# Kernel tuning notes

Measured on AMD Instinct MI355X. Metric: run time of the kernel, lower is better.

## Reference

```python
import jax, jax.numpy as jnp
import numpy as np

EMBED = 1024
N_HEAD = 16
D_HID = EMBED // N_HEAD
R_FF = 4
D_FF = EMBED * R_FF
LN_EPS = 1e-5


def layer_norm(x, gamma, beta):
    mu = jnp.mean(x, axis=-1, keepdims=True)
    var = jnp.var(x, axis=-1, keepdims=True)
    return (x - mu) * jax.lax.rsqrt(var + LN_EPS) * gamma + beta


def setup_inputs() -> dict:
    key = jax.random.key(0)
    ks = jax.random.split(key, 10)
    B, S = 4, 2048
    # torch nn.Linear stores weight as [out, in]; y = x @ W.T
    def xavier(k, shape):
        fan_out, fan_in = shape
        lim = np.sqrt(6.0 / (fan_in + fan_out))
        return jax.random.uniform(k, shape, jnp.float32, -lim, lim)
    return {
        "x": jax.random.normal(ks[0], (B, S, EMBED), jnp.float32),
        "Wq": xavier(ks[1], (EMBED, EMBED)),
        "Wk": xavier(ks[2], (EMBED, EMBED)),
        "Wv": xavier(ks[3], (EMBED, EMBED)),
        "Wo": xavier(ks[4], (EMBED, EMBED)),
        "bo": jnp.zeros((EMBED,), jnp.float32),
        "ln1_g": jnp.ones((EMBED,), jnp.float32),
        "ln1_b": jnp.zeros((EMBED,), jnp.float32),
        "ln2_g": jnp.ones((EMBED,), jnp.float32),
        "ln2_b": jnp.zeros((EMBED,), jnp.float32),
        "W1": jax.random.normal(ks[5], (D_FF, EMBED), jnp.float32) * np.sqrt(2.0 / EMBED),
        "b1": jnp.zeros((D_FF,), jnp.float32),
        "W2": xavier(ks[6], (EMBED, D_FF)),
        "b2": jnp.zeros((EMBED,), jnp.float32),
    }


def reference(x, Wq, Wk, Wv, Wo, bo, ln1_g, ln1_b, ln2_g, ln2_b, W1, b1, W2, b2):
    B, S, E = x.shape
    scaling = 1.0 / np.sqrt(D_HID)
    # --- attention (pre-LN), dropout = identity (eval) ---
    xn = layer_norm(x, ln1_g, ln1_b)
    q = (xn @ Wq.T).reshape(B, S, N_HEAD, D_HID) * scaling
    k = (xn @ Wk.T).reshape(B, S, N_HEAD, D_HID)
    v = (xn @ Wv.T).reshape(B, S, N_HEAD, D_HID)
    scores = jnp.einsum("bqhd,bkhd->bhqk", q, k)
    attn = jax.nn.softmax(scores, axis=-1)
    out = jnp.einsum("bhqk,bkhd->bqhd", attn, v).reshape(B, S, E)
    out = out @ Wo.T + bo
    x = x + out
    # --- feed-forward (pre-LN) ---
    xn = layer_norm(x, ln2_g, ln2_b)
    h = jax.nn.relu(xn @ W1.T + b1)
    x = x + (h @ W2.T + b2)
    return x
```

## Files before the change

kernel.cpp:

```cpp
#include <hip/hip_runtime.h>
#include <hip/hip_bf16.h>
#include <cstdint>


typedef __attribute__((ext_vector_type(8))) short bf16x8;
typedef __attribute__((ext_vector_type(4))) float f32x4;

#define LDSAS __attribute__((address_space(3)))
#define GLBAS __attribute__((address_space(1)))

#define CQK 0.18033688011112044f

__device__ __forceinline__ unsigned short f2bf(float f) {
  union { float f; unsigned u; } c; c.f = f;
  unsigned u = c.u + 0x7fffu + ((c.u >> 16) & 1u);
  return (unsigned short)(u >> 16);
}

__device__ __forceinline__ unsigned pk2(float a, float b) {
  __hip_bfloat162 h = __float22bfloat162_rn(make_float2(a, b));
  union { __hip_bfloat162 h; unsigned u; } c; c.h = h; return c.u;
}

__device__ __forceinline__ void async16(const unsigned short* g, unsigned short* l) {
  __builtin_amdgcn_global_load_lds((const GLBAS unsigned int*)g,
                                   (LDSAS unsigned int*)l, 16, 0, 0);
}

__global__ void cvt_all(const float* __restrict__ q, const float* __restrict__ k,
                        const float* __restrict__ v, const float* __restrict__ o,
                        const float* __restrict__ w1, const float* __restrict__ w2,
                        unsigned short* __restrict__ wsb) {
  const long i = (long)blockIdx.x * 256 + threadIdx.x;
  const float* src; unsigned short* dst; long off;
  if (i < 1048576) {
    const long seg = i >> 18, o4 = i & 262143;
    src = (seg == 0) ? q : (seg == 1) ? k : (seg == 2) ? v : o;
    dst = wsb + ((seg == 3) ? 3145728L : seg * 1048576L);
    off = o4;
  } else if (i < 2097152) {
    src = w1; dst = wsb + 4194304; off = i - 1048576;
  } else {
    src = w2; dst = wsb + 8388608; off = i - 2097152;
  }
  const float4 vv = ((const float4*)src)[off];
  ushort4 r;
  r.x = f2bf(vv.x); r.y = f2bf(vv.y); r.z = f2bf(vv.z); r.w = f2bf(vv.w);
  ((ushort4*)dst)[off] = r;
}

__global__ void ln_fwd(const float* __restrict__ x, const float* __restrict__ g,
                       const float* __restrict__ bb, unsigned short* __restrict__ outp) {
  const int row = blockIdx.x, tid = threadIdx.x;
  const float4 v = ((const float4*)(x + (long)row * 1024))[tid];
  float s  = v.x + v.y + v.z + v.w;
  float sq = v.x * v.x + v.y * v.y + v.z * v.z + v.w * v.w;
#pragma unroll
  for (int off = 1; off < 64; off <<= 1) {
    s  += __shfl_xor(s, off);
    sq += __shfl_xor(sq, off);
  }
  __shared__ float red[8];
  const int wv = tid >> 6, lane = tid & 63;
  if (lane == 0) { red[wv] = s; red[4 + wv] = sq; }
  __syncthreads();
  s  = red[0] + red[1] + red[2] + red[3];
  sq = red[4] + red[5] + red[6] + red[7];
  const float mu  = s * (1.f / 1024.f);
  const float var = sq * (1.f / 1024.f) - mu * mu;
  const float rstd = rsqrtf(var + 1e-5f);
  const float4 gv = ((const float4*)g)[tid];
  const float4 bv = ((const float4*)bb)[tid];
  ushort4 o;
  o.x = f2bf((v.x - mu) * rstd * gv.x + bv.x);
  o.y = f2bf((v.y - mu) * rstd * gv.y + bv.y);
  o.z = f2bf((v.z - mu) * rstd * gv.z + bv.z);
  o.w = f2bf((v.w - mu) * rstd * gv.w + bv.w);
  ((ushort4*)(outp + (long)row * 1024))[tid] = o;
}

template <int EPI>
__launch_bounds__(256, 3)
__global__ void gemm_bt(const unsigned short* __restrict__ A,
                        const unsigned short* __restrict__ B,
                        void* __restrict__ Cout,
                        const float* __restrict__ bias,
                        const float* __restrict__ res,
                        int M, int N, int K) {
  __shared__ __align__(16) unsigned short As[128 * 64];
  __shared__ __align__(16) unsigned short Bs[128 * 64];
  const int tid  = threadIdx.x;
  const int lane = tid & 63;
  const int wvu  = __builtin_amdgcn_readfirstlane(tid >> 6);
  const int quad = lane >> 4, l16 = lane & 15;
  const int wm = wvu >> 1, wn = wvu & 1;

  const int gx = gridDim.x;
  const int id = blockIdx.y * gx + blockIdx.x;
  const int xcd = id & 7, slot = id >> 3;
  const int by = xcd * 8 + (slot & 7);
  const int bx = slot >> 3;
  const long m0 = (long)by * 128, n0 = (long)bx * 128;

  f32x4 acc[4][4];
#pragma unroll
  for (int i = 0; i < 4; i++)
#pragma unroll
    for (int j = 0; j < 4; j++) acc[i][j] = (f32x4){0.f, 0.f, 0.f, 0.f};

  const int rxA = l16 & 7;
  const int c0A = quad ^ rxA;
  int srow[4], sgc[4];
#pragma unroll
  for (int j = 0; j < 4; ++j) {
    const int s = wvu * 256 + j * 64 + lane;
    srow[j] = s >> 3;
    sgc[j] = ((s & 7) ^ (srow[j] & 7)) * 8;
  }

  for (int k0 = 0; k0 < K; k0 += 64) {
    __syncthreads();
#pragma unroll
    for (int j = 0; j < 4; ++j) {
      const int db = (wvu * 256 + j * 64) * 8;
      async16(A + (m0 + srow[j]) * K + k0 + sgc[j], As + db);
      async16(B + (n0 + srow[j]) * K + k0 + sgc[j], Bs + db);
    }
    __syncthreads();

#pragma unroll
    for (int kc = 0; kc < 2; ++kc) {
      const int ch = (c0A ^ (kc * 4)) * 8;
      bf16x8 af[4], bfr[4];
#pragma unroll
      for (int t = 0; t < 4; ++t) {
        af[t]  = *(const bf16x8*)(As + (wm * 64 + t * 16 + l16) * 64 + ch);
        bfr[t] = *(const bf16x8*)(Bs + (wn * 64 + t * 16 + l16) * 64 + ch);
      }
#pragma unroll
      for (int mt = 0; mt < 4; ++mt)
#pragma unroll
        for (int nt = 0; nt < 4; ++nt)
          acc[mt][nt] = __builtin_amdgcn_mfma_f32_16x16x32_bf16(af[mt], bfr[nt],
                                                                acc[mt][nt], 0, 0, 0);
    }
  }

#pragma unroll
  for (int nt = 0; nt < 4; ++nt) {
    const long col = n0 + wn * 64 + nt * 16 + l16;
    float bv = 0.f;
    if (EPI == 1 || EPI == 2) bv = bias[col];
    const float scl = (EPI == 3 && col < 1024) ? CQK : 1.0f;
#pragma unroll
    for (int mt = 0; mt < 4; ++mt) {
#pragma unroll
      for (int r = 0; r < 4; ++r) {
        const long row = m0 + wm * 64 + mt * 16 + quad * 4 + r;
        const long idx = row * (long)N + col;
        float v = acc[mt][nt][r];
        if (EPI == 0) {
          ((unsigned short*)Cout)[idx] = f2bf(v);
        } else if (EPI == 1) {
          ((float*)Cout)[idx] = v + bv + res[idx];
        } else if (EPI == 2) {
          v += bv;
          ((unsigned short*)Cout)[idx] = f2bf(v > 0.f ? v : 0.f);
        } else {
          ((unsigned short*)Cout)[idx] = f2bf(v * scl);
        }
      }
    }
  }
}

__global__ void vprep(const unsigned short* __restrict__ qkv,
                      unsigned short* __restrict__ vt) {
  __shared__ unsigned short T[64 * 68];
  const int tid = threadIdx.x;
  const int t = blockIdx.x;
  const int bh = blockIdx.y;
  const int b = bh >> 4, h = bh & 15;
  const long base = ((long)b * 2048 + t * 64) * 3072 + 2048 + h * 64;
#pragma unroll
  for (int i = 0; i < 4; ++i) {
    int c = i * 256 + tid;
    int r = c >> 4, d4 = (c & 15) * 4;
    *(ushort4*)(T + r * 68 + d4) = *(const ushort4*)(qkv + base + (long)r * 3072 + d4);
  }
  __syncthreads();
  unsigned short* out = vt + ((long)bh * 32 + t) * 4096;
#pragma unroll
  for (int i = 0; i < 4; ++i) {
    int u = i * 256 + tid;
    int c = u >> 1, half = u & 1;
    int d = c >> 3;
    int k = ((c & 7) - d) & 7;
    int kvp4 = k * 8 + half * 4;
    int sk = (kvp4 & 32) | ((kvp4 & 4) << 2) | ((kvp4 & 16) >> 1) | ((kvp4 & 8) >> 1);
    ushort4 o;
    o.x = T[(sk + 0) * 68 + d];
    o.y = T[(sk + 1) * 68 + d];
    o.z = T[(sk + 2) * 68 + d];
    o.w = T[(sk + 3) * 68 + d];
    *(ushort4*)(out + u * 4) = o;
  }
}

__launch_bounds__(256, 2)
__global__ void attn_fwd(const unsigned short* __restrict__ qkv,
                         const unsigned short* __restrict__ vt,
                         unsigned short* __restrict__ outp) {
  __shared__ __align__(16) unsigned short lds[32768];

  const int tid = threadIdx.x;
  const int lane = tid & 63;
  const int wv = __builtin_amdgcn_readfirstlane(tid >> 6);
  const int quad = lane >> 4, l16 = lane & 15;

  const int id = blockIdx.y * 16 + blockIdx.x;
  const int xcd = id & 7, slot = id >> 3;
  const int bh = xcd * 8 + (slot >> 4);
  const int qt = slot & 15;
  const int b = bh >> 4, h = bh & 15;
  const long rowbase = (long)b * 2048;
  const int hoff = h * 64;

  unsigned short* Qs = lds + 16384;

  {
    const unsigned short* qsrc = qkv + (rowbase + qt * 128) * 3072 + hoff;
#pragma unroll
    for (int j = 0; j < 4; ++j) {
      const int c = j * 256 + wv * 64 + lane;
      const int row = c >> 3;
      const int k = ((c & 7) - row) & 7;
      async16(qsrc + (long)row * 3072 + k * 8, Qs + (j * 256 + wv * 64) * 8);
    }
  }
  asm volatile("s_waitcnt vmcnt(0)" ::: "memory");
  __builtin_amdgcn_s_barrier();
  __builtin_amdgcn_sched_barrier(0);

  const int rot0 = (quad + l16) & 7;
  const int rot1 = rot0 ^ 4;

  bf16x8 bq[2][2];
#pragma unroll
  for (int s = 0; s < 2; ++s) {
    const int qrow = wv * 32 + s * 16 + l16;
    bq[s][0] = *(const bf16x8*)(Qs + qrow * 64 + rot0 * 8);
    bq[s][1] = *(const bf16x8*)(Qs + qrow * 64 + rot1 * 8);
  }
  asm volatile("s_waitcnt lgkmcnt(0)" ::: "memory");
  __builtin_amdgcn_sched_barrier(0);
  __builtin_amdgcn_s_barrier();
  __builtin_amdgcn_sched_barrier(0);

  const int c0 = wv * 64 + lane;
  const int r0 = c0 >> 3;
  const int ks = ((c0 & 7) - r0) & 7;
  const unsigned short* kptr = qkv + (rowbase + r0) * 3072 + 1024 + hoff + ks * 8;
  const unsigned short* vptr = vt + (long)bh * 131072 + (long)c0 * 8;

  auto stage = [&](int t) {
    unsigned short* kdst = lds + (t & 1) * 16384 + wv * 512;
    unsigned short* vdst = kdst + 8192;
    const unsigned short* kp = kptr + (long)t * 128 * 3072;
    const unsigned short* vp = vptr + (long)t * 8192;
#pragma unroll
    for (int j = 0; j < 4; ++j) {
      async16(kp + (long)j * 32 * 3072, kdst + j * 2048);
      async16(vp + j * 2048, vdst + j * 2048);
    }
  };

  bf16x8 ones;
#pragma unroll
  for (int i = 0; i < 8; ++i) ones[i] = (short)0x3F80;

  f32x4 oacc[2][4], lacc[2];
#pragma unroll
  for (int s = 0; s < 2; ++s) {
    lacc[s] = (f32x4){0.f, 0.f, 0.f, 0.f};
#pragma unroll
    for (int i = 0; i < 4; ++i) oacc[s][i] = (f32x4){0.f, 0.f, 0.f, 0.f};
  }

  stage(0); stage(1);
  asm volatile("s_waitcnt vmcnt(8)" ::: "memory");
  __builtin_amdgcn_s_barrier();
  __builtin_amdgcn_sched_barrier(0);

  for (int kt = 0; kt < 16; ++kt) {
    const unsigned short* Kb = lds + (kt & 1) * 16384;
    const unsigned short* Vb = Kb + 8192;

    f32x4 sacc[2][8];
#pragma unroll
    for (int t = 0; t < 8; ++t) {
      const int ar = t * 16 + l16;
      bf16x8 ak0 = *(const bf16x8*)(Kb + ar * 64 + rot0 * 8);
      bf16x8 ak1 = *(const bf16x8*)(Kb + ar * 64 + rot1 * 8);
#pragma unroll
      for (int s = 0; s < 2; ++s) {
        f32x4 z = (f32x4){0.f, 0.f, 0.f, 0.f};
        z = __builtin_amdgcn_mfma_f32_16x16x32_bf16(ak0, bq[s][0], z, 0, 0, 0);
        sacc[s][t] = __builtin_amdgcn_mfma_f32_16x16x32_bf16(ak1, bq[s][1], z, 0, 0, 0);
      }
    }

    union APU { unsigned u[4]; bf16x8 v; } ap[2][4];
#pragma unroll
    for (int s = 0; s < 2; ++s)
#pragma unroll
      for (int hf = 0; hf < 4; ++hf) {
#pragma unroll
        for (int t = 0; t < 2; ++t) {
          const f32x4 sv = sacc[s][hf * 2 + t];
          const float p0 = __builtin_amdgcn_exp2f(sv[0]);
          const float p1 = __builtin_amdgcn_exp2f(sv[1]);
          const float p2 = __builtin_amdgcn_exp2f(sv[2]);
          const float p3 = __builtin_amdgcn_exp2f(sv[3]);
          ap[s][hf].u[t * 2 + 0] = pk2(p0, p1);
          ap[s][hf].u[t * 2 + 1] = pk2(p2, p3);
        }
        lacc[s] = __builtin_amdgcn_mfma_f32_16x16x32_bf16(ap[s][hf].v, ones,
                                                          lacc[s], 0, 0, 0);
      }

#pragma unroll
    for (int hf = 0; hf < 4; ++hf) {
      const int vbase = (hf >> 1) * 4096 + ((hf & 1) ? rot1 : rot0) * 8;
#pragma unroll
      for (int dt = 0; dt < 4; ++dt) {
        bf16x8 bv = *(const bf16x8*)(Vb + vbase + (dt * 16 + l16) * 64);
#pragma unroll
        for (int s = 0; s < 2; ++s)
          oacc[s][dt] = __builtin_amdgcn_mfma_f32_16x16x32_bf16(ap[s][hf].v, bv,
                                                                oacc[s][dt], 0, 0, 0);
      }
    }

    if (kt == 15) break;
    __builtin_amdgcn_s_barrier();
    __builtin_amdgcn_sched_barrier(0);
    if (kt + 2 < 16) {
      stage(kt + 2);
      asm volatile("s_waitcnt vmcnt(8)" ::: "memory");
    } else {
      asm volatile("s_waitcnt vmcnt(0)" ::: "memory");
    }
    __builtin_amdgcn_s_barrier();
    __builtin_amdgcn_sched_barrier(0);
  }

#pragma unroll
  for (int s = 0; s < 2; ++s) {
    float linv[4];
#pragma unroll
    for (int r = 0; r < 4; ++r) linv[r] = 1.f / lacc[s][r];
#pragma unroll
    for (int dt = 0; dt < 4; ++dt)
#pragma unroll
      for (int r = 0; r < 4; ++r) {
        const long row = rowbase + qt * 128 + wv * 32 + s * 16 + quad * 4 + r;
        outp[row * 1024 + hoff + dt * 16 + l16] = f2bf(oacc[s][dt][r] * linv[r]);
      }
  }
}

extern "C" void kernel_launch(void* const* d_in, const int* in_sizes, int n_in,
                              void* d_out, int out_size, void* d_ws, size_t ws_size,
                              hipStream_t stream) {
  (void)in_sizes; (void)n_in; (void)out_size; (void)ws_size;
  const float* x   = (const float*)d_in[0];
  const float* Wq  = (const float*)d_in[1];
  const float* Wk  = (const float*)d_in[2];
  const float* Wv  = (const float*)d_in[3];
  const float* Wo  = (const float*)d_in[4];
  const float* bo  = (const float*)d_in[5];
  const float* g1  = (const float*)d_in[6];
  const float* be1 = (const float*)d_in[7];
  const float* g2  = (const float*)d_in[8];
  const float* be2 = (const float*)d_in[9];
  const float* W1  = (const float*)d_in[10];
  const float* bf1 = (const float*)d_in[11];
  const float* W2  = (const float*)d_in[12];
  const float* bf2 = (const float*)d_in[13];

  char* ws = (char*)d_ws;
  unsigned short* wqkv  = (unsigned short*)(ws);
  unsigned short* wo    = (unsigned short*)(ws + 6291456);
  unsigned short* w1    = (unsigned short*)(ws + 8388608);
  unsigned short* w2    = (unsigned short*)(ws + 16777216);
  unsigned short* xn    = (unsigned short*)(ws + 25165824);
  unsigned short* big   = (unsigned short*)(ws + 41943040);
  unsigned short* attnb = (unsigned short*)(ws + 109051904);
  float*          x1    = (float*)(ws + 125829120);
  unsigned short* vtg   = xn;

  cvt_all<<<12288, 256, 0, stream>>>(Wq, Wk, Wv, Wo, W1, W2, wqkv);

  ln_fwd<<<8192, 256, 0, stream>>>(x, g1, be1, xn);
  gemm_bt<3><<<dim3(24, 64), 256, 0, stream>>>(xn, wqkv, big, nullptr, nullptr,
                                               8192, 3072, 1024);
  vprep<<<dim3(32, 64), 256, 0, stream>>>(big, vtg);
  attn_fwd<<<dim3(16, 64), 256, 0, stream>>>(big, vtg, attnb);
  gemm_bt<1><<<dim3(8, 64), 256, 0, stream>>>(attnb, wo, x1, bo, x,
                                              8192, 1024, 1024);
  ln_fwd<<<8192, 256, 0, stream>>>(x1, g2, be2, xn);
  gemm_bt<2><<<dim3(32, 64), 256, 0, stream>>>(xn, w1, big, bf1, nullptr,
                                               8192, 4096, 1024);
  gemm_bt<1><<<dim3(8, 64), 256, 0, stream>>>(big, w2, (float*)d_out, bf2, x1,
                                              8192, 1024, 4096);
}
```

Before: 490.8 us.

## Halve attention KV tile to raise occupancy, load Q directly, add setprio

The attention kernel now stages 64-key K/V tiles instead of 128, which halves LDS use and allows four blocks per CU instead of two. Q fragments are loaded straight from global memory into registers, so the Q LDS staging and its barriers are gone. MFMA phases are wrapped in s_setprio so waves doing matrix work get priority over waves doing softmax. The cost is twice as many loop iterations and barriers, and a tighter register budget under the new launch bounds.

```diff
diff --git a/kernel.cpp b/kernel.cpp
--- a/kernel.cpp
+++ b/kernel.cpp
@@ -207,11 +207,11 @@
   }
 }
 
-__launch_bounds__(256, 2)
+__launch_bounds__(256, 4)
 __global__ void attn_fwd(const unsigned short* __restrict__ qkv,
                          const unsigned short* __restrict__ vt,
                          unsigned short* __restrict__ outp) {
-  __shared__ __align__(16) unsigned short lds[32768];
+  __shared__ __align__(16) unsigned short lds[16384];
 
   const int tid = threadIdx.x;
   const int lane = tid & 63;
@@ -226,35 +226,17 @@
   const long rowbase = (long)b * 2048;
   const int hoff = h * 64;
 
-  unsigned short* Qs = lds + 16384;
-
-  {
-    const unsigned short* qsrc = qkv + (rowbase + qt * 128) * 3072 + hoff;
-#pragma unroll
-    for (int j = 0; j < 4; ++j) {
-      const int c = j * 256 + wv * 64 + lane;
-      const int row = c >> 3;
-      const int k = ((c & 7) - row) & 7;
-      async16(qsrc + (long)row * 3072 + k * 8, Qs + (j * 256 + wv * 64) * 8);
-    }
-  }
-  asm volatile("s_waitcnt vmcnt(0)" ::: "memory");
-  __builtin_amdgcn_s_barrier();
-  __builtin_amdgcn_sched_barrier(0);
-
   const int rot0 = (quad + l16) & 7;
   const int rot1 = rot0 ^ 4;
 
   bf16x8 bq[2][2];
 #pragma unroll
   for (int s = 0; s < 2; ++s) {
-    const int qrow = wv * 32 + s * 16 + l16;
-    bq[s][0] = *(const bf16x8*)(Qs + qrow * 64 + rot0 * 8);
-    bq[s][1] = *(const bf16x8*)(Qs + qrow * 64 + rot1 * 8);
-  }
-  asm volatile("s_waitcnt lgkmcnt(0)" ::: "memory");
-  __builtin_amdgcn_sched_barrier(0);
-  __builtin_amdgcn_s_barrier();
+    const long qrow = rowbase + qt * 128 + wv * 32 + s * 16 + l16;
+    const unsigned short* qp = qkv + qrow * 3072 + hoff;
+    bq[s][0] = *(const bf16x8*)(qp + quad * 8);
+    bq[s][1] = *(const bf16x8*)(qp + (quad ^ 4) * 8);
+  }
   __builtin_amdgcn_sched_barrier(0);
 
   const int c0 = wv * 64 + lane;
@@ -264,12 +246,12 @@
   const unsigned short* vptr = vt + (long)bh * 131072 + (long)c0 * 8;
 
   auto stage = [&](int t) {
-    unsigned short* kdst = lds + (t & 1) * 16384 + wv * 512;
-    unsigned short* vdst = kdst + 8192;
-    const unsigned short* kp = kptr + (long)t * 128 * 3072;
-    const unsigned short* vp = vptr + (long)t * 8192;
-#pragma unroll
-    for (int j = 0; j < 4; ++j) {
+    unsigned short* kdst = lds + (t & 1) * 4096 + wv * 512;
+    unsigned short* vdst = lds + 8192 + (t & 1) * 4096 + wv * 512;
+    const unsigned short* kp = kptr + (long)t * 64 * 3072;
+    const unsigned short* vp = vptr + (long)t * 4096;
+#pragma unroll
+    for (int j = 0; j < 2; ++j) {
       async16(kp + (long)j * 32 * 3072, kdst + j * 2048);
       async16(vp + j * 2048, vdst + j * 2048);
     }
@@ -288,17 +270,18 @@
   }
 
   stage(0); stage(1);
-  asm volatile("s_waitcnt vmcnt(8)" ::: "memory");
+  asm volatile("s_waitcnt vmcnt(4)" ::: "memory");
   __builtin_amdgcn_s_barrier();
   __builtin_amdgcn_sched_barrier(0);
 
-  for (int kt = 0; kt < 16; ++kt) {
-    const unsigned short* Kb = lds + (kt & 1) * 16384;
-    const unsigned short* Vb = Kb + 8192;
-
-    f32x4 sacc[2][8];
-#pragma unroll
-    for (int t = 0; t < 8; ++t) {
+  for (int kt = 0; kt < 32; ++kt) {
+    const unsigned short* Kb = lds + (kt & 1) * 4096;
+    const unsigned short* Vb = lds + 8192 + (kt & 1) * 4096;
+
+    f32x4 sacc[2][4];
+    __builtin_amdgcn_s_setprio(1);
+#pragma unroll
+    for (int t = 0; t < 4; ++t) {
       const int ar = t * 16 + l16;
       bf16x8 ak0 = *(const bf16x8*)(Kb + ar * 64 + rot0 * 8);
       bf16x8 ak1 = *(const bf16x8*)(Kb + ar * 64 + rot1 * 8);
@@ -309,12 +292,13 @@
         sacc[s][t] = __builtin_amdgcn_mfma_f32_16x16x32_bf16(ak1, bq[s][1], z, 0, 0, 0);
       }
     }
-
-    union APU { unsigned u[4]; bf16x8 v; } ap[2][4];
+    __builtin_amdgcn_s_setprio(0);
+
+    union APU { unsigned u[4]; bf16x8 v; } ap[2][2];
 #pragma unroll
     for (int s = 0; s < 2; ++s)
 #pragma unroll
-      for (int hf = 0; hf < 4; ++hf) {
+      for (int hf = 0; hf < 2; ++hf) {
 #pragma unroll
         for (int t = 0; t < 2; ++t) {
           const f32x4 sv = sacc[s][hf * 2 + t];
@@ -329,9 +313,10 @@
                                                           lacc[s], 0, 0, 0);
       }
 
-#pragma unroll
-    for (int hf = 0; hf < 4; ++hf) {
-      const int vbase = (hf >> 1) * 4096 + ((hf & 1) ? rot1 : rot0) * 8;
+    __builtin_amdgcn_s_setprio(1);
+#pragma unroll
+    for (int hf = 0; hf < 2; ++hf) {
+      const int vbase = (hf ? rot1 : rot0) * 8;
 #pragma unroll
       for (int dt = 0; dt < 4; ++dt) {
         bf16x8 bv = *(const bf16x8*)(Vb + vbase + (dt * 16 + l16) * 64);
@@ -341,13 +326,14 @@
                                                                 oacc[s][dt], 0, 0, 0);
       }
     }
-
-    if (kt == 15) break;
+    __builtin_amdgcn_s_setprio(0);
+
+    if (kt == 31) break;
     __builtin_amdgcn_s_barrier();
     __builtin_amdgcn_sched_barrier(0);
-    if (kt + 2 < 16) {
+    if (kt + 2 < 32) {
       stage(kt + 2);
-      asm volatile("s_waitcnt vmcnt(8)" ::: "memory");
+      asm volatile("s_waitcnt vmcnt(4)" ::: "memory");
     } else {
       asm volatile("s_waitcnt vmcnt(0)" ::: "memory");
     }
```

Measured after the change: 485.3 us. Within noise of the previous version (-1.1%).
